# Performance work log

Hardware: AMD Instinct MI355X
Metric: run time of the kernel (lower is better)

The kernel has to match this reference:

```python
import jax, jax.numpy as jnp
import numpy as np

N_EMBD = 1024
N_HEAD = 16
B, T = 4, 2048


def setup_inputs() -> dict:
    key = jax.random.key(0)
    ks = jax.random.split(key, 9)
    s = 1.0 / np.sqrt(N_EMBD)
    def lin(k):
        kw, kb = jax.random.split(k)
        W = jax.random.uniform(kw, (N_EMBD, N_EMBD), jnp.float32, -s, s)
        b = jax.random.uniform(kb, (N_EMBD,), jnp.float32, -s, s)
        return W, b
    Wq, bq = lin(ks[0])
    Wk, bk = lin(ks[1])
    Wv, bv = lin(ks[2])
    Wc, bc = lin(ks[3])
    x = jax.random.normal(ks[4], (B, T, N_EMBD), jnp.float32)
    return {"x": x, "Wq": Wq, "bq": bq, "Wk": Wk, "bk": bk,
            "Wv": Wv, "bv": bv, "Wc": Wc, "bc": bc}


def reference(x, Wq, bq, Wk, bk, Wv, bv, Wc, bc):
    Bsz, Tlen, C = x.shape
    hd = C // N_HEAD  # head dim
    # projections (torch Linear: x @ W.T + b)
    q = x @ Wq.T + bq
    k = x @ Wk.T + bk
    v = x @ Wv.T + bv
    # [B, H, T, hd]
    q = q.reshape(Bsz, Tlen, N_HEAD, hd).transpose(0, 2, 1, 3)
    k = k.reshape(Bsz, Tlen, N_HEAD, hd).transpose(0, 2, 1, 3)
    v = v.reshape(Bsz, Tlen, N_HEAD, hd).transpose(0, 2, 1, 3)
    scale = 1.0 / np.sqrt(hd).astype(np.float32)
    att = jnp.einsum('bhqd,bhkd->bhqk', q, k) * scale  # [B,H,T,T]
    causal = jnp.tril(jnp.ones((Tlen, Tlen), dtype=bool))
    att = jnp.where(causal[None, None, :, :], att, -jnp.inf)
    att = jax.nn.softmax(att, axis=-1)
    y = jnp.einsum('bhqk,bhkd->bhqd', att, v)  # [B,H,T,hd]
    y = y.transpose(0, 2, 1, 3).reshape(Bsz, Tlen, C)
    return y @ Wc.T + bc
```

## Files before the change

### kernel.cpp

```cpp
#include <hip/hip_runtime.h>
#include <hip/hip_bf16.h>

typedef __bf16 bf16x8 __attribute__((ext_vector_type(8)));
typedef float f32x4 __attribute__((ext_vector_type(4)));
typedef unsigned short u16;
typedef u16 u16x8 __attribute__((ext_vector_type(8)));
typedef unsigned int u32;
typedef u32 u32x4 __attribute__((ext_vector_type(4)));

#define N_EMBD 1024
#define NH 16
#define HD 64
#define BZ 4
#define TZ 2048
#define QSCALE 0.18033688011f

template<bool B> struct BoolC { static constexpr bool value = B; };

__device__ __forceinline__ u16 f2bf(float f) {
    return __builtin_bit_cast(u16, (__bf16)f);
}

__device__ __forceinline__ void gload16(const void* g, void* l) {
    __builtin_amdgcn_global_load_lds(
        (const __attribute__((address_space(1))) void*)g,
        (__attribute__((address_space(3))) void*)l, 16, 0, 0);
}

__global__ void cvt_f32_bf16(const float* __restrict__ src, u16* __restrict__ dst,
                             int n4, float scale) {
    int i = blockIdx.x * blockDim.x + threadIdx.x;
    if (i < n4) {
        float4 f = ((const float4*)src)[i];
        ushort4 o;
        o.x = f2bf(f.x * scale); o.y = f2bf(f.y * scale);
        o.z = f2bf(f.z * scale); o.w = f2bf(f.w * scale);
        ((ushort4*)dst)[i] = o;
    }
}

template<int EPI>
__global__ __launch_bounds__(512, 2) void gemm_bt(
    const u16* __restrict__ A, const u16* __restrict__ Bm,
    const float* __restrict__ b0, const float* __restrict__ b1, const float* __restrict__ b2,
    void* __restrict__ Cout, int K) {
    __shared__ __align__(16) u16 Ash[6 * 8192];
    __shared__ __align__(16) u16 Bsh[6 * 4096];

    const int tid = threadIdx.x;
    const int lane = tid & 63, wid = tid >> 6;
    const int wm = wid >> 1, wn = wid & 1;
    const int m0 = blockIdx.x * 256, n0 = blockIdx.y * 128;
    const int r = lane & 15, g = lane >> 4;

    f32x4 acc[4][4] = {};

    const int p0 = tid >> 3;
    const int ci = tid & 7;
    const int cl = ci ^ (p0 & 7);
    const int trow = 2 * p0 + (cl >> 2);
    const int colb = (cl & 3) * 8;
    const u16* aS = A + (long)(m0 + trow) * K + colb;
    const u16* bS = Bm + (long)(n0 + trow) * K + colb;
    const long rowskip = (long)128 * K;
    const int ldst = tid * 8;

    auto STAGE = [&](int sig, int kq) {
        const u16* spA = aS + kq * 32;
        gload16(spA, &Ash[sig * 8192 + ldst]);
        gload16(spA + rowskip, &Ash[sig * 8192 + 4096 + ldst]);
        gload16(bS + kq * 32, &Bsh[sig * 4096 + ldst]);
    };

    const int xa = (((((r & 1) << 2) | g) ^ (r >> 1)) << 4);
    const int arow0 = wm * 32 + (r >> 1);
    const int brow0 = wn * 32 + (r >> 1);
    auto RD = [&](const u16* base, int prow) -> bf16x8 {
        return *(const bf16x8*)((const char*)base + prow * 128 + xa);
    };

    bf16x8 fa0[4], fb0[4], fa1[4], fb1[4];

    auto READF = [&](int rho, bf16x8* fa, bf16x8* fb) {
#pragma unroll
        for (int m = 0; m < 4; ++m) fa[m] = RD(&Ash[rho * 8192], arow0 + m * 8);
#pragma unroll
        for (int n = 0; n < 4; ++n) fb[n] = RD(&Bsh[rho * 4096], brow0 + n * 8);
    };
    auto MM = [&](bf16x8* fa, bf16x8* fb) {
        __builtin_amdgcn_s_setprio(1);
#pragma unroll
        for (int m = 0; m < 4; ++m)
#pragma unroll
            for (int n = 0; n < 4; ++n)
                acc[m][n] = __builtin_amdgcn_mfma_f32_16x16x32_bf16(fa[m], fb[n], acc[m][n], 0, 0, 0);
        __builtin_amdgcn_s_setprio(0);
    };
    auto BAR = [&] {
        asm volatile("" ::: "memory");
        __builtin_amdgcn_s_barrier();
        asm volatile("" ::: "memory");
    };

    const int nph = K >> 5;

    STAGE(0, 0); STAGE(1, 1); STAGE(2, 2); STAGE(3, 3); STAGE(4, 4);
    asm volatile("s_waitcnt vmcnt(9)" ::: "memory");
    BAR();
    READF(0, fa0, fb0);

    int rho = 0;
    for (int p = 0; p + 2 < nph; p += 2) {
        const int rho1 = rho + 1;
        const int rho2 = (rho + 2 == 6) ? 0 : rho + 2;
        const int sigE = (rho == 0) ? 5 : rho - 1;
        const int kqE = (p + 5 < nph) ? p + 5 : 0;
        const int kqO = (p + 6 < nph) ? p + 6 : 0;
        BAR();
        READF(rho1, fa1, fb1);
        STAGE(sigE, kqE);
        MM(fa0, fb0);
        asm volatile("s_waitcnt vmcnt(9)" ::: "memory");
        BAR();
        READF(rho2, fa0, fb0);
        STAGE(rho, kqO);
        MM(fa1, fb1);
        asm volatile("s_waitcnt vmcnt(9)" ::: "memory");
        rho = rho2;
    }
    {
        const int rho1 = rho + 1;
        const int sigE = (rho == 0) ? 5 : rho - 1;
        BAR();
        READF(rho1, fa1, fb1);
        STAGE(sigE, 0);
        MM(fa0, fb0);
        asm volatile("s_waitcnt vmcnt(9)" ::: "memory");
    }
    MM(fa1, fb1);
    asm volatile("s_waitcnt vmcnt(0)" ::: "memory");

    const long planeSz = (long)BZ * NH * TZ * HD;
    if constexpr (EPI == 0) {
        const int proj = n0 >> 10;
        u16* outp = (u16*)Cout;
        if (proj == 2) {
            const int bi = (m0 + wm * 64) >> 11;
#pragma unroll
            for (int n = 0; n < 4; ++n) {
                const int rr = (n0 & 1023) + wn * 64 + n * 16 + r;
                const int h = rr >> 6, d = rr & 63;
                const float bias = b2[rr];
                u16* vcol = outp + 2 * planeSz + (((long)bi * NH + h) * HD + d) * TZ;
#pragma unroll
                for (int m = 0; m < 4; ++m) {
                    const int t0 = (m0 + wm * 64 + m * 16 + g * 4) & 2047;
                    ushort4 o;
                    o.x = f2bf(acc[m][n][0] + bias);
                    o.y = f2bf(acc[m][n][1] + bias);
                    o.z = f2bf(acc[m][n][2] + bias);
                    o.w = f2bf(acc[m][n][3] + bias);
                    *(ushort4*)(vcol + t0) = o;
                }
            }
        } else {
#pragma unroll
            for (int n = 0; n < 4; ++n) {
                const int rr = (n0 & 1023) + wn * 64 + n * 16 + r;
                const int h = rr >> 6, d = rr & 63;
                float bias = (proj == 0 ? b0 : b1)[rr];
                if (proj == 0) bias *= QSCALE;
                const long pbase = (long)proj * planeSz + d;
#pragma unroll
                for (int m = 0; m < 4; ++m)
#pragma unroll
                    for (int reg = 0; reg < 4; ++reg) {
                        const int row = m0 + wm * 64 + m * 16 + g * 4 + reg;
                        const int bi = row >> 11, t = row & 2047;
                        outp[pbase + ((long)bi * NH + h) * (TZ * HD) + (long)t * HD] =
                            f2bf(acc[m][n][reg] + bias);
                    }
            }
        }
    } else {
        float* outp = (float*)Cout;
#pragma unroll
        for (int n = 0; n < 4; ++n) {
            const int col = n0 + wn * 64 + n * 16 + r;
            const float bias = b0[col];
#pragma unroll
            for (int m = 0; m < 4; ++m)
#pragma unroll
                for (int reg = 0; reg < 4; ++reg) {
                    const int row = m0 + wm * 64 + m * 16 + g * 4 + reg;
                    outp[(long)row * N_EMBD + col] = acc[m][n][reg] + bias;
                }
        }
    }
}

__device__ __forceinline__ bf16x8 lds_swz8(const u16* base, int row, int colByte) {
    return *(const bf16x8*)((const char*)base + row * 128 + (colByte ^ ((row & 7) << 4)));
}

__global__ __launch_bounds__(256, 4) void attn_fwd(const u16* __restrict__ qkv, u16* __restrict__ yb) {
    const int i = blockIdx.x;
    const int xcd = i & 7, slot = i >> 3;
    const int bh = xcd + 8 * (slot & 7);
    const int pr = slot >> 3;
    const int b = bh >> 4, h = bh & 15;
    const int tid = threadIdx.x, lane = tid & 63, w = tid >> 6;
    const int r = lane & 15, g = lane >> 4;

    __shared__ __align__(16) u16 Ksh[2][64 * 64];
    __shared__ __align__(16) u16 Vsh[2][64 * 64];

    const long planeSz = (long)BZ * NH * TZ * HD;
    const long bhoff = ((long)b * NH + h) * (long)TZ * HD;
    const u16* qp = qkv + bhoff;
    const u16* kp = qkv + planeSz + bhoff;
    const u16* vTp = qkv + 2 * planeSz + bhoff;

    const int rr8 = tid >> 3, scb = tid & 7;

#pragma unroll 1
    for (int it = 0; it < 2; ++it) {
        const int qblk = it ? pr : (31 - pr);
        const int q0 = qblk * 64;
        const int nkt = qblk + 1;

        bf16x8 qf[2];
        {
            const int q = q0 + w * 16 + r;
#pragma unroll
            for (int ks = 0; ks < 2; ++ks)
                qf[ks] = *(const bf16x8*)(qp + (long)q * HD + ks * 32 + g * 8);
        }

        f32x4 yacc[4] = {};
        float mrun = -__builtin_inff(), lpart = 0.f;

#pragma unroll
        for (int h2 = 0; h2 < 2; ++h2) {
            const int kk = h2 * 32 + rr8;
            const int ss = (scb ^ (kk & 7)) * 8;
            gload16(kp + (long)kk * HD + ss, &Ksh[0][h2 * 2048 + tid * 8]);
            gload16(vTp + (long)kk * TZ + ss, &Vsh[0][h2 * 2048 + tid * 8]);
        }

        auto tile = [&](int kt, auto maskc) {
            constexpr bool MASK = decltype(maskc)::value;
            const int cur = kt & 1;
            const int k0 = kt * 64;
            if (kt + 1 < nkt) {
                const int k0n = k0 + 64;
#pragma unroll
                for (int h2 = 0; h2 < 2; ++h2) {
                    const int kk = h2 * 32 + rr8;
                    const int ss = (scb ^ (kk & 7)) * 8;
                    gload16(kp + (long)(k0n + kk) * HD + ss, &Ksh[cur ^ 1][h2 * 2048 + tid * 8]);
                    gload16(vTp + (long)kk * TZ + k0n + ss, &Vsh[cur ^ 1][h2 * 2048 + tid * 8]);
                }
                asm volatile("s_waitcnt vmcnt(4)" ::: "memory");
            } else {
                asm volatile("s_waitcnt vmcnt(0)" ::: "memory");
            }
            __builtin_amdgcn_s_barrier();
            asm volatile("" ::: "memory");

            f32x4 sac[4] = {};
#pragma unroll
            for (int ks = 0; ks < 2; ++ks) {
                bf16x8 kf[4];
#pragma unroll
                for (int nk = 0; nk < 4; ++nk)
                    kf[nk] = lds_swz8(Ksh[cur], nk * 16 + r, ks * 64 + g * 16);
                __builtin_amdgcn_s_setprio(1);
#pragma unroll
                for (int nk = 0; nk < 4; ++nk)
                    sac[nk] = __builtin_amdgcn_mfma_f32_16x16x32_bf16(kf[nk], qf[ks], sac[nk], 0, 0, 0);
                __builtin_amdgcn_s_setprio(0);
            }

            if constexpr (MASK) {
                const int q = q0 + w * 16 + r;
#pragma unroll
                for (int nk = 0; nk < 4; ++nk)
#pragma unroll
                    for (int reg = 0; reg < 4; ++reg) {
                        const int k = k0 + nk * 16 + g * 4 + reg;
                        sac[nk][reg] = (k > q) ? -__builtin_inff() : sac[nk][reg];
                    }
            }
            float pmax;
            {
                float t0 = fmaxf(fmaxf(sac[0][0], sac[0][1]), fmaxf(sac[0][2], sac[0][3]));
                float t1 = fmaxf(fmaxf(sac[1][0], sac[1][1]), fmaxf(sac[1][2], sac[1][3]));
                float t2 = fmaxf(fmaxf(sac[2][0], sac[2][1]), fmaxf(sac[2][2], sac[2][3]));
                float t3 = fmaxf(fmaxf(sac[3][0], sac[3][1]), fmaxf(sac[3][2], sac[3][3]));
                pmax = fmaxf(fmaxf(t0, t1), fmaxf(t2, t3));
            }
            if (__any(pmax > mrun + 8.0f)) {
                float mx = pmax;
                mx = fmaxf(mx, __shfl_xor(mx, 16));
                mx = fmaxf(mx, __shfl_xor(mx, 32));
                const float mnew = fmaxf(mrun, mx);
                const float corr = __builtin_amdgcn_exp2f(mrun - mnew);
                lpart *= corr;
#pragma unroll
                for (int nd = 0; nd < 4; ++nd)
                    yacc[nd] *= corr;
                mrun = mnew;
            }
            float rs[4];
#pragma unroll
            for (int nk = 0; nk < 4; ++nk) {
                float p0 = __builtin_amdgcn_exp2f(sac[nk][0] - mrun);
                float p1 = __builtin_amdgcn_exp2f(sac[nk][1] - mrun);
                float p2 = __builtin_amdgcn_exp2f(sac[nk][2] - mrun);
                float p3 = __builtin_amdgcn_exp2f(sac[nk][3] - mrun);
                sac[nk][0] = p0; sac[nk][1] = p1;
                sac[nk][2] = p2; sac[nk][3] = p3;
                rs[nk] = (p0 + p1) + (p2 + p3);
            }
            lpart += (rs[0] + rs[1]) + (rs[2] + rs[3]);

            u32 wv[4][2];
#pragma unroll
            for (int nk = 0; nk < 4; ++nk)
#pragma unroll
                for (int j2 = 0; j2 < 2; ++j2)
                    asm("v_cvt_pk_bf16_f32 %0, %1, %2"
                        : "=v"(wv[nk][j2])
                        : "v"(sac[nk][2 * j2]), "v"(sac[nk][2 * j2 + 1]));
            u32 pw[2][4];
#pragma unroll
            for (int ks = 0; ks < 2; ++ks) {
                u32 a0 = wv[2 * ks][0], b0 = wv[2 * ks + 1][0];
                u32 a1 = wv[2 * ks][1], b1 = wv[2 * ks + 1][1];
                asm("v_permlane32_swap_b32 %0, %1" : "+v"(a0), "+v"(b0));
                asm("v_permlane32_swap_b32 %0, %1" : "+v"(a1), "+v"(b1));
                asm("v_permlane16_swap_b32 %0, %1" : "+v"(a0), "+v"(b0));
                asm("v_permlane16_swap_b32 %0, %1" : "+v"(a1), "+v"(b1));
                pw[ks][0] = a0; pw[ks][1] = a1;
                pw[ks][2] = b0; pw[ks][3] = b1;
            }

#pragma unroll
            for (int ks = 0; ks < 2; ++ks) {
                bf16x8 vf[4];
#pragma unroll
                for (int nd = 0; nd < 4; ++nd)
                    vf[nd] = lds_swz8(Vsh[cur], nd * 16 + r, ks * 64 + g * 16);
                const u32x4 pwv = { pw[ks][0], pw[ks][1], pw[ks][2], pw[ks][3] };
                const bf16x8 pb = __builtin_bit_cast(bf16x8, pwv);
                __builtin_amdgcn_s_setprio(1);
#pragma unroll
                for (int nd = 0; nd < 4; ++nd)
                    yacc[nd] = __builtin_amdgcn_mfma_f32_16x16x32_bf16(vf[nd], pb, yacc[nd], 0, 0, 0);
                __builtin_amdgcn_s_setprio(0);
            }

            asm volatile("" ::: "memory");
            __builtin_amdgcn_s_barrier();
            asm volatile("" ::: "memory");
        };

        for (int kt = 0; kt < nkt - 1; ++kt) tile(kt, BoolC<false>{});
        tile(nkt - 1, BoolC<true>{});

        {
            float l = lpart;
            l += __shfl_xor(l, 16);
            l += __shfl_xor(l, 32);
            const float inv = 1.f / l;
            const int q = q0 + w * 16 + r;
            u16* orow = yb + ((long)b * TZ + q) * N_EMBD + h * HD;
#pragma unroll
            for (int nd = 0; nd < 4; ++nd) {
                ushort4 o;
                o.x = f2bf(yacc[nd][0] * inv);
                o.y = f2bf(yacc[nd][1] * inv);
                o.z = f2bf(yacc[nd][2] * inv);
                o.w = f2bf(yacc[nd][3] * inv);
                *(ushort4*)(orow + nd * 16 + g * 4) = o;
            }
        }
    }
}

extern "C" void kernel_launch(void* const* d_in, const int* in_sizes, int n_in,
                              void* d_out, int out_size, void* d_ws, size_t ws_size,
                              hipStream_t stream) {
    const float* x  = (const float*)d_in[0];
    const float* Wq = (const float*)d_in[1];
    const float* bq = (const float*)d_in[2];
    const float* Wk = (const float*)d_in[3];
    const float* bk = (const float*)d_in[4];
    const float* Wv = (const float*)d_in[5];
    const float* bv = (const float*)d_in[6];
    const float* Wc = (const float*)d_in[7];
    const float* bc = (const float*)d_in[8];

    char* ws = (char*)d_ws;
    u16* xb   = (u16*)(ws);
    u16* wqkv = (u16*)(ws + 16777216);
    u16* wcb  = (u16*)(ws + 23068672);
    u16* qkv  = (u16*)(ws + 25165824);
    u16* yb   = (u16*)(ws + 75497472);

    cvt_f32_bf16<<<8192, 256, 0, stream>>>(x, xb, 2097152, 1.0f);
    cvt_f32_bf16<<<1024, 256, 0, stream>>>(Wq, wqkv, 262144, QSCALE);
    cvt_f32_bf16<<<1024, 256, 0, stream>>>(Wk, wqkv + 1048576, 262144, 1.0f);
    cvt_f32_bf16<<<1024, 256, 0, stream>>>(Wv, wqkv + 2097152, 262144, 1.0f);
    cvt_f32_bf16<<<1024, 256, 0, stream>>>(Wc, wcb, 262144, 1.0f);

    gemm_bt<0><<<dim3(32, 24), 512, 0, stream>>>(xb, wqkv, bq, bk, bv, (void*)qkv, 1024);

    attn_fwd<<<1024, 256, 0, stream>>>(qkv, yb);

    gemm_bt<1><<<dim3(32, 8), 512, 0, stream>>>(yb, wcb, bc, nullptr, nullptr, d_out, 1024);
}
```

Baseline: 169.4 us.

## Use 128-query attention blocks with 8 waves and fuse conversion launches

The five f32-to-bf16 conversion launches are merged into a single kernel that picks its source by block index, removing launch overhead. The attention kernel moves to 512-thread blocks covering 128 query rows, so each loaded 64-key K/V tile is shared by 8 waves instead of 4, halving K/V traffic per query. Each thread now issues one load per operand per tile, and the last two tiles both use the masked path. The grid is halved to 512 blocks, which may reduce load balance and occupancy flexibility.

```diff
diff --git a/kernel.cpp b/kernel.cpp
--- a/kernel.cpp
+++ b/kernel.cpp
@@ -27,16 +27,23 @@
         (__attribute__((address_space(3))) void*)l, 16, 0, 0);
 }
 
-__global__ void cvt_f32_bf16(const float* __restrict__ src, u16* __restrict__ dst,
-                             int n4, float scale) {
-    int i = blockIdx.x * blockDim.x + threadIdx.x;
-    if (i < n4) {
-        float4 f = ((const float4*)src)[i];
-        ushort4 o;
-        o.x = f2bf(f.x * scale); o.y = f2bf(f.y * scale);
-        o.z = f2bf(f.z * scale); o.w = f2bf(f.w * scale);
-        ((ushort4*)dst)[i] = o;
-    }
+__global__ void cvt_all(const float* __restrict__ x,  const float* __restrict__ Wq,
+                        const float* __restrict__ Wk, const float* __restrict__ Wv,
+                        const float* __restrict__ Wc, u16* __restrict__ xb,
+                        u16* __restrict__ wqkv, u16* __restrict__ wcb) {
+    const int blk = blockIdx.x;
+    const float* src; u16* dst; int base; float scale = 1.0f;
+    if (blk < 8192)       { src = x;  dst = xb;             base = blk; }
+    else if (blk < 9216)  { src = Wq; dst = wqkv;           base = blk - 8192; scale = QSCALE; }
+    else if (blk < 10240) { src = Wk; dst = wqkv + 1048576; base = blk - 9216; }
+    else if (blk < 11264) { src = Wv; dst = wqkv + 2097152; base = blk - 10240; }
+    else                  { src = Wc; dst = wcb;            base = blk - 11264; }
+    const int i = base * 256 + threadIdx.x;
+    float4 f = ((const float4*)src)[i];
+    ushort4 o;
+    o.x = f2bf(f.x * scale); o.y = f2bf(f.y * scale);
+    o.z = f2bf(f.z * scale); o.w = f2bf(f.w * scale);
+    ((ushort4*)dst)[i] = o;
 }
 
 template<int EPI>
@@ -203,7 +210,7 @@
     return *(const bf16x8*)((const char*)base + row * 128 + (colByte ^ ((row & 7) << 4)));
 }
 
-__global__ __launch_bounds__(256, 4) void attn_fwd(const u16* __restrict__ qkv, u16* __restrict__ yb) {
+__global__ __launch_bounds__(512, 2) void attn_fwd(const u16* __restrict__ qkv, u16* __restrict__ yb) {
     const int i = blockIdx.x;
     const int xcd = i & 7, slot = i >> 3;
     const int bh = xcd + 8 * (slot & 7);
@@ -221,13 +228,14 @@
     const u16* kp = qkv + planeSz + bhoff;
     const u16* vTp = qkv + 2 * planeSz + bhoff;
 
-    const int rr8 = tid >> 3, scb = tid & 7;
+    const int rr8 = tid >> 3;
+    const int ss = ((tid & 7) ^ (rr8 & 7)) * 8;
 
 #pragma unroll 1
     for (int it = 0; it < 2; ++it) {
-        const int qblk = it ? pr : (31 - pr);
-        const int q0 = qblk * 64;
-        const int nkt = qblk + 1;
+        const int qblk = it ? pr : (15 - pr);
+        const int q0 = qblk * 128;
+        const int nkt = 2 * qblk + 2;
 
         bf16x8 qf[2];
         {
@@ -240,13 +248,8 @@
         f32x4 yacc[4] = {};
         float mrun = -__builtin_inff(), lpart = 0.f;
 
-#pragma unroll
-        for (int h2 = 0; h2 < 2; ++h2) {
-            const int kk = h2 * 32 + rr8;
-            const int ss = (scb ^ (kk & 7)) * 8;
-            gload16(kp + (long)kk * HD + ss, &Ksh[0][h2 * 2048 + tid * 8]);
-            gload16(vTp + (long)kk * TZ + ss, &Vsh[0][h2 * 2048 + tid * 8]);
-        }
+        gload16(kp + (long)rr8 * HD + ss, &Ksh[0][tid * 8]);
+        gload16(vTp + (long)rr8 * TZ + ss, &Vsh[0][tid * 8]);
 
         auto tile = [&](int kt, auto maskc) {
             constexpr bool MASK = decltype(maskc)::value;
@@ -254,14 +257,9 @@
             const int k0 = kt * 64;
             if (kt + 1 < nkt) {
                 const int k0n = k0 + 64;
-#pragma unroll
-                for (int h2 = 0; h2 < 2; ++h2) {
-                    const int kk = h2 * 32 + rr8;
-                    const int ss = (scb ^ (kk & 7)) * 8;
-                    gload16(kp + (long)(k0n + kk) * HD + ss, &Ksh[cur ^ 1][h2 * 2048 + tid * 8]);
-                    gload16(vTp + (long)kk * TZ + k0n + ss, &Vsh[cur ^ 1][h2 * 2048 + tid * 8]);
-                }
-                asm volatile("s_waitcnt vmcnt(4)" ::: "memory");
+                gload16(kp + (long)(k0n + rr8) * HD + ss, &Ksh[cur ^ 1][tid * 8]);
+                gload16(vTp + (long)rr8 * TZ + k0n + ss, &Vsh[cur ^ 1][tid * 8]);
+                asm volatile("s_waitcnt vmcnt(2)" ::: "memory");
             } else {
                 asm volatile("s_waitcnt vmcnt(0)" ::: "memory");
             }
@@ -366,7 +364,8 @@
             asm volatile("" ::: "memory");
         };
 
-        for (int kt = 0; kt < nkt - 1; ++kt) tile(kt, BoolC<false>{});
+        for (int kt = 0; kt + 2 < nkt; ++kt) tile(kt, BoolC<false>{});
+        tile(nkt - 2, BoolC<true>{});
         tile(nkt - 1, BoolC<true>{});
 
         {
@@ -409,15 +408,11 @@
     u16* qkv  = (u16*)(ws + 25165824);
     u16* yb   = (u16*)(ws + 75497472);
 
-    cvt_f32_bf16<<<8192, 256, 0, stream>>>(x, xb, 2097152, 1.0f);
-    cvt_f32_bf16<<<1024, 256, 0, stream>>>(Wq, wqkv, 262144, QSCALE);
-    cvt_f32_bf16<<<1024, 256, 0, stream>>>(Wk, wqkv + 1048576, 262144, 1.0f);
-    cvt_f32_bf16<<<1024, 256, 0, stream>>>(Wv, wqkv + 2097152, 262144, 1.0f);
-    cvt_f32_bf16<<<1024, 256, 0, stream>>>(Wc, wcb, 262144, 1.0f);
+    cvt_all<<<12288, 256, 0, stream>>>(x, Wq, Wk, Wv, Wc, xb, wqkv, wcb);
 
     gemm_bt<0><<<dim3(32, 24), 512, 0, stream>>>(xb, wqkv, bq, bk, bv, (void*)qkv, 1024);
 
-    attn_fwd<<<1024, 256, 0, stream>>>(qkv, yb);
+    attn_fwd<<<512, 512, 0, stream>>>(qkv, yb);
 
     gemm_bt<1><<<dim3(32, 8), 512, 0, stream>>>(yb, wcb, bc, nullptr, nullptr, d_out, 1024);
 }
```

After: 161.5 us. 1.05x faster.
